# Kernel optimization log

Measured on AMD Instinct MI355X. Metric: run time of the kernel, lower is better.

## Reference

```python
import jax, jax.numpy as jnp
import numpy as np

EPS = 1e-7
ATTN_W_EPS = float(np.sqrt(EPS))
RESIDUAL_SCALE = 1.0


def mish(v):
    return v * jnp.tanh(jax.nn.softplus(v))


def setup_inputs() -> dict:
    key = jax.random.key(0)
    ks = jax.random.split(key, 12)
    N, E, dim, hidden = 100000, 500000, 128, 128
    x = jax.random.normal(ks[0], (N, dim), dtype=jnp.float32)
    edge_attr = jax.random.normal(ks[1], (E, dim), dtype=jnp.float32)
    head_node_index = jax.random.randint(ks[2], (E,), 0, N)
    tail_node_index = jax.random.randint(ks[3], (E,), 0, N)
    node_batch = jax.random.randint(ks[4], (N,), 0, 8)
    edge_batch = jax.random.randint(ks[5], (E,), 0, 8)
    s_in = 1.0 / np.sqrt(dim)
    s_out = 1.0 / np.sqrt(hidden)
    W_node_in = jax.random.normal(ks[6], (dim, 4 * hidden), dtype=jnp.float32) * s_in
    W_edge_in = jax.random.normal(ks[7], (dim, 3 * hidden), dtype=jnp.float32) * s_in
    node_message_bias = jnp.zeros((hidden,), dtype=jnp.float32)
    edge_message_bias = jnp.zeros((hidden,), dtype=jnp.float32)
    W_node_out = jax.random.normal(ks[8], (hidden, dim), dtype=jnp.float32) * s_out
    b_node_out = jnp.zeros((dim,), dtype=jnp.float32)
    W_edge_out = jax.random.normal(ks[9], (hidden, dim), dtype=jnp.float32) * s_out
    b_edge_out = jnp.zeros((dim,), dtype=jnp.float32)
    return {
        'x': x, 'edge_attr': edge_attr,
        'head_node_index': head_node_index, 'tail_node_index': tail_node_index,
        'node_batch': node_batch, 'edge_batch': edge_batch,
        'num_nodes': N, 'num_graphs': 8,
        'W_node_in': W_node_in, 'W_edge_in': W_edge_in,
        'node_message_bias': node_message_bias, 'edge_message_bias': edge_message_bias,
        'W_node_out': W_node_out, 'b_node_out': b_node_out,
        'W_edge_out': W_edge_out, 'b_edge_out': b_edge_out,
    }


def reference(x, edge_attr, head_node_index, tail_node_index, node_batch, edge_batch,
              num_nodes, num_graphs, W_node_in, W_edge_in,
              node_message_bias, edge_message_bias,
              W_node_out, b_node_out, W_edge_out, b_edge_out):
    hidden = node_message_bias.shape[0]
    # node input linear -> 4 chunks
    node_messages = x @ W_node_in  # [N, 4*hidden]
    node_to_self, node_to_neighbor, head_to_edge, tail_to_edge = jnp.split(node_messages, 4, axis=-1)
    node_to_edge = head_to_edge[head_node_index] + tail_to_edge[tail_node_index]  # [E, hidden]
    # edge input linear -> 3 chunks
    edge_messages = edge_attr @ W_edge_in  # [E, 3*hidden]
    edge_to_self, edge_to_tail, edge_attn_message = jnp.split(edge_messages, 3, axis=-1)
    # segment-softmax-style attention weight (max detached, per tail node)
    seg_max = jax.ops.segment_max(jax.lax.stop_gradient(edge_attn_message), tail_node_index,
                                  num_segments=num_nodes)  # [N, hidden]
    edge_attn_weight = jnp.exp(edge_attn_message - seg_max[tail_node_index]) + ATTN_W_EPS  # [E, hidden]
    # attention-weighted scatter aggregation to tail nodes
    sent = (node_to_neighbor[head_node_index] + edge_to_tail) * edge_attn_weight  # [E, hidden]
    received = jax.ops.segment_sum(sent, tail_node_index, num_segments=num_nodes)
    recv_weight = jax.ops.segment_sum(edge_attn_weight, tail_node_index, num_segments=num_nodes)
    node_received = received / (recv_weight + EPS)  # [N, hidden]
    # node output path
    x_residual = mish(node_received + node_to_self + node_message_bias) @ W_node_out + b_node_out
    x_out = x + RESIDUAL_SCALE * x_residual
    # edge output path
    e_residual = mish(node_to_edge + edge_to_self + edge_message_bias) @ W_edge_out + b_edge_out
    edge_attr_out = edge_attr + RESIDUAL_SCALE * e_residual
    return (x_out, edge_attr_out)
```

## Files before the change

kernel.cpp:

```cpp
#include <hip/hip_runtime.h>
#include <hip/hip_bf16.h>
#include <math.h>

typedef short bf16x8 __attribute__((ext_vector_type(8)));
typedef float f32x4 __attribute__((ext_vector_type(4)));
typedef unsigned int u32;
typedef unsigned short u16;

#define DIM 128
#define ATTN_EPS 3.1622776601683794e-4f
#define DIV_EPS 1e-7f
#define SCAN_BLKS 256

__device__ __forceinline__ u16 f2b(float f) {
  u32 u = __float_as_uint(f);
  return (u16)((u + 0x7FFFu + ((u >> 16) & 1u)) >> 16);
}
__device__ __forceinline__ float b2f(u16 s) { return __uint_as_float(((u32)s) << 16); }
__device__ __forceinline__ float mish_f(float v) {
  float e = __expf(fminf(v, 15.f));
  float w = 1.f + e;
  return v * (1.f - 2.f * __builtin_amdgcn_rcpf(w * w + 1.f));
}

template <int NT, int NR>
__device__ __forceinline__ void stage_f32(u16 (*dst)[136], const float* __restrict__ src,
                                          long rowbase, long nrows, int tid) {
  #pragma unroll
  for (int it = 0; it < NR * 16 / NT; ++it) {
    int i = it * NT + tid;
    int r = i >> 4, c = (i & 15) * 8;
    long gr = rowbase + r;
    bf16x8 v;
    if (gr < nrows) {
      const f32x4* p = (const f32x4*)(src + gr * (long)DIM + c);
      f32x4 a = p[0], b = p[1];
      #pragma unroll
      for (int j = 0; j < 4; ++j) { v[j] = (short)f2b(a[j]); v[j + 4] = (short)f2b(b[j]); }
    } else {
      #pragma unroll
      for (int j = 0; j < 8; ++j) v[j] = 0;
    }
    *(bf16x8*)&dst[r][c] = v;
  }
}

template <int NT, int NR>
__device__ __forceinline__ void stage_b16(u16 (*dst)[136], const u16* __restrict__ src, int tid) {
  #pragma unroll
  for (int it = 0; it < NR * 16 / NT; ++it) {
    int i = it * NT + tid;
    int r = i >> 4, c = (i & 15) * 8;
    *(bf16x8*)&dst[r][c] = *(const bf16x8*)&src[(long)r * DIM + c];
  }
}

template <int NT, int NR>
__device__ __forceinline__ void gather_nm(u16 (*dst)[136], const u16* __restrict__ nm,
    const int* __restrict__ idx, int segoff, long rowbase, long nrows, int tid) {
  #pragma unroll
  for (int it = 0; it < NR * 16 / NT; ++it) {
    int i = it * NT + tid;
    int r = i >> 4, c = (i & 15) * 8;
    long gr = rowbase + r;
    bf16x8 v;
    if (gr < nrows) {
      v = *(const bf16x8*)&nm[(long)idx[gr] * 512 + segoff + c];
    } else {
      #pragma unroll
      for (int j = 0; j < 8; ++j) v[j] = 0;
    }
    *(bf16x8*)&dst[r][c] = v;
  }
}

__device__ __forceinline__ void mm_32x64(const u16 (*As)[136], const u16 (*Bs)[136],
                                         int wr, int wc, int lane, f32x4 acc[2][4]) {
  int r0 = wr * 32 + (lane & 15);
  int cb = wc * 64 + (lane & 15);
  int koff = (lane >> 4) * 8;
  #pragma unroll
  for (int ks = 0; ks < 4; ++ks) {
    int k = ks * 32 + koff;
    bf16x8 a0 = *(const bf16x8*)&As[r0][k];
    bf16x8 a1 = *(const bf16x8*)&As[r0 + 16][k];
    #pragma unroll
    for (int ct = 0; ct < 4; ++ct) {
      bf16x8 b = *(const bf16x8*)&Bs[cb + ct * 16][k];
      acc[0][ct] = __builtin_amdgcn_mfma_f32_16x16x32_bf16(a0, b, acc[0][ct], 0, 0, 0);
      acc[1][ct] = __builtin_amdgcn_mfma_f32_16x16x32_bf16(a1, b, acc[1][ct], 0, 0, 0);
    }
  }
}

__global__ void k_prep(const float* __restrict__ Wni, const float* __restrict__ Wei,
                       const float* __restrict__ Wno, const float* __restrict__ Weo,
                       u16* __restrict__ Tni, u16* __restrict__ Tei,
                       u16* __restrict__ Tno, u16* __restrict__ Teo) {
  int stride = gridDim.x * blockDim.x;
  int t0 = blockIdx.x * blockDim.x + threadIdx.x;
  for (int i = t0; i < 128 * 512; i += stride) { int k = i >> 9, c = i & 511; Tni[c * 128 + k] = f2b(Wni[i]); }
  for (int i = t0; i < 128 * 384; i += stride) { int k = i / 384, c = i % 384; Tei[c * 128 + k] = f2b(Wei[i]); }
  for (int i = t0; i < 128 * 128; i += stride) { int k = i >> 7, c = i & 127; Tno[c * 128 + k] = f2b(Wno[i]); }
  for (int i = t0; i < 128 * 128; i += stride) { int k = i >> 7, c = i & 127; Teo[c * 128 + k] = f2b(Weo[i]); }
}

__global__ __launch_bounds__(256) void k_node_in(const float* __restrict__ x,
    const u16* __restrict__ Tni, u16* __restrict__ nm, int N) {
  __shared__ u16 As[64][136];
  __shared__ u16 Bs[128][136];
  int tid = threadIdx.x, lane = tid & 63;
  int wid = tid >> 6, wr = wid >> 1, wc = wid & 1;
  long rowbase = (long)blockIdx.x * 64;
  stage_f32<256, 64>(As, x, rowbase, N, tid);
  stage_b16<256, 128>(Bs, Tni + (long)blockIdx.y * 128 * DIM, tid);
  __syncthreads();
  f32x4 acc[2][4] = {};
  mm_32x64(As, Bs, wr, wc, lane, acc);
  #pragma unroll
  for (int rt = 0; rt < 2; ++rt)
  #pragma unroll
  for (int j = 0; j < 4; ++j) {
    int lr = wr * 32 + rt * 16 + ((lane >> 4) << 2) + j;
    long r = rowbase + lr;
    if (r >= N) continue;
    #pragma unroll
    for (int ct = 0; ct < 4; ++ct) {
      int col = blockIdx.y * 128 + wc * 64 + ct * 16 + (lane & 15);
      nm[r * 512 + col] = f2b(acc[rt][ct][j]);
    }
  }
}

__global__ __launch_bounds__(512, 4) void k_edge_in(const float* __restrict__ ea,
    const u16* __restrict__ Tei, const u16* __restrict__ Teo,
    const u16* __restrict__ nm, const int* __restrict__ head, const int* __restrict__ tail,
    const float* __restrict__ ebias, const float* __restrict__ beo,
    u32* __restrict__ em, float* __restrict__ eout, int E) {
  __shared__ u16 As[128][136];
  __shared__ u16 Bs[128][136];
  int tid = threadIdx.x, lane = tid & 63;
  int wid = tid >> 6, wr = wid >> 1, wc = wid & 1;
  long rowbase = (long)blockIdx.x * 128;
  int col0 = wc * 64 + (lane & 15);

  stage_f32<512, 128>(As, ea, rowbase, E, tid);
  stage_b16<512, 128>(Bs, Tei + 128 * DIM, tid);
  __syncthreads();
  f32x4 acc_t[2][4] = {};
  mm_32x64(As, Bs, wr, wc, lane, acc_t);
  __syncthreads();
  stage_b16<512, 128>(Bs, Tei + 256 * DIM, tid);
  __syncthreads();
  f32x4 acc_m[2][4] = {};
  mm_32x64(As, Bs, wr, wc, lane, acc_m);
  __syncthreads();
  gather_nm<512, 128>(Bs, nm, head, 128, rowbase, E, tid);
  __syncthreads();
  #pragma unroll
  for (int rt = 0; rt < 2; ++rt)
  #pragma unroll
  for (int j = 0; j < 4; ++j) {
    int lr = wr * 32 + rt * 16 + ((lane >> 4) << 2) + j;
    long r = rowbase + lr;
    if (r < E) {
      #pragma unroll
      for (int ct = 0; ct < 4; ++ct) {
        int col = col0 + ct * 16;
        float n2n = b2f(Bs[lr][col]);
        em[r * 128 + col] = (u32)f2b(n2n + acc_t[rt][ct][j])
                          | ((u32)f2b(acc_m[rt][ct][j]) << 16);
      }
    }
  }
  __syncthreads();
  stage_b16<512, 128>(Bs, Tei, tid);
  __syncthreads();
  f32x4 acc_s[2][4] = {};
  mm_32x64(As, Bs, wr, wc, lane, acc_s);
  __syncthreads();
  gather_nm<512, 128>(Bs, nm, head, 256, rowbase, E, tid);
  gather_nm<512, 128>(As, nm, tail, 384, rowbase, E, tid);
  __syncthreads();
  #pragma unroll
  for (int rt = 0; rt < 2; ++rt)
  #pragma unroll
  for (int j = 0; j < 4; ++j) {
    int lr = wr * 32 + rt * 16 + ((lane >> 4) << 2) + j;
    long r = rowbase + lr;
    #pragma unroll
    for (int ct = 0; ct < 4; ++ct) {
      int col = col0 + ct * 16;
      if (r < E) {
        float epre = acc_s[rt][ct][j] + b2f(Bs[lr][col]) + b2f(As[lr][col]) + ebias[col];
        As[lr][col] = f2b(mish_f(epre));
      } else {
        As[lr][col] = 0;
      }
    }
  }
  __syncthreads();
  stage_b16<512, 128>(Bs, Teo, tid);
  __syncthreads();
  f32x4 acc_o[2][4] = {};
  mm_32x64(As, Bs, wr, wc, lane, acc_o);
  #pragma unroll
  for (int rt = 0; rt < 2; ++rt)
  #pragma unroll
  for (int j = 0; j < 4; ++j) {
    int lr = wr * 32 + rt * 16 + ((lane >> 4) << 2) + j;
    long r = rowbase + lr;
    if (r >= E) continue;
    #pragma unroll
    for (int ct = 0; ct < 4; ++ct) {
      int col = col0 + ct * 16;
      eout[r * DIM + col] = ea[r * DIM + col] + acc_o[rt][ct][j] + beo[col];
    }
  }
}

__global__ void k_zero(u32* __restrict__ deg, int N) {
  int i = blockIdx.x * blockDim.x + threadIdx.x;
  int stride = gridDim.x * blockDim.x;
  for (; i < N; i += stride) deg[i] = 0;
}
__global__ void k_count(const int* __restrict__ tail, u32* __restrict__ deg, int E) {
  int i = blockIdx.x * blockDim.x + threadIdx.x;
  int stride = gridDim.x * blockDim.x;
  for (; i < E; i += stride) atomicAdd(&deg[tail[i]], 1u);
}
__global__ __launch_bounds__(256) void k_scan_part(const u32* __restrict__ deg,
                                                   u32* __restrict__ part, int N) {
  __shared__ u32 red[256];
  int tid = threadIdx.x, b = blockIdx.x;
  int chunk = (N + SCAN_BLKS - 1) / SCAN_BLKS;
  int lo = b * chunk, hi = min(lo + chunk, N);
  u32 s = 0;
  for (int i = lo + tid; i < hi; i += 256) s += deg[i];
  red[tid] = s; __syncthreads();
  for (int st = 128; st > 0; st >>= 1) { if (tid < st) red[tid] += red[tid + st]; __syncthreads(); }
  if (tid == 0) part[b] = red[0];
}
__global__ __launch_bounds__(256) void k_scan_mid(u32* __restrict__ part) {
  __shared__ u32 lds[256];
  int tid = threadIdx.x;
  u32 v = part[tid];
  lds[tid] = v; __syncthreads();
  for (int s = 1; s < 256; s <<= 1) {
    u32 a = (tid >= s) ? lds[tid - s] : 0; __syncthreads();
    lds[tid] += a; __syncthreads();
  }
  part[tid] = lds[tid] - v;
}
__global__ __launch_bounds__(256) void k_scan_fin(const u32* __restrict__ deg,
    const u32* __restrict__ part, u32* __restrict__ off, u32* __restrict__ cur, int N) {
  __shared__ u32 lds[256];
  int tid = threadIdx.x, b = blockIdx.x;
  int chunk = (N + SCAN_BLKS - 1) / SCAN_BLKS;
  int lo = b * chunk, hi = min(lo + chunk, N);
  u32 carry = part[b];
  for (int base = lo; base < hi; base += 256) {
    int i = base + tid;
    u32 v = (i < hi) ? deg[i] : 0;
    lds[tid] = v; __syncthreads();
    for (int s = 1; s < 256; s <<= 1) {
      u32 a = (tid >= s) ? lds[tid - s] : 0; __syncthreads();
      lds[tid] += a; __syncthreads();
    }
    u32 incl = lds[tid], total = lds[255];
    __syncthreads();
    if (i < hi) { u32 o = carry + incl - v; off[i] = o; cur[i] = o; }
    carry += total;
  }
}
__global__ void k_fill(const int* __restrict__ tail, u32* __restrict__ cur,
                       u32* __restrict__ csr, int E) {
  int i = blockIdx.x * blockDim.x + threadIdx.x;
  int stride = gridDim.x * blockDim.x;
  for (; i < E; i += stride) { u32 p = atomicAdd(&cur[tail[i]], 1u); csr[p] = (u32)i; }
}

__global__ __launch_bounds__(256) void k_node_agg(const u32* __restrict__ em,
    const u16* __restrict__ nm, const u32* __restrict__ off, const u32* __restrict__ deg,
    const u32* __restrict__ csr, const float* __restrict__ nbias,
    u16* __restrict__ hbuf, int N) {
  int tid = threadIdx.x, lane = tid & 63;
  int node = blockIdx.x * 4 + (tid >> 6);
  if (node >= N) return;
  int ch = lane * 2;
  u32 o = off[node], d = deg[node];
  float m0 = -INFINITY, m1 = -INFINITY;
  float s0 = 0.f, s1 = 0.f, v0 = 0.f, v1 = 0.f, sv0 = 0.f, sv1 = 0.f;
  u32 e = d ? csr[o] : 0u;
  for (u32 i = 0; i < d; ++i) {
    u32 ec = e;
    if (i + 1 < d) e = csr[o + i + 1];
    uint2 pp = *(const uint2*)(em + (long)ec * 128 + ch);
    float val0 = b2f((u16)(pp.x & 0xffff)), g0 = b2f((u16)(pp.x >> 16));
    float val1 = b2f((u16)(pp.y & 0xffff)), g1 = b2f((u16)(pp.y >> 16));
    float nmx0 = fmaxf(m0, g0);
    float sc0 = __expf(m0 - nmx0), pe0 = __expf(g0 - nmx0);
    s0 = s0 * sc0 + pe0; v0 = v0 * sc0 + pe0 * val0; sv0 += val0; m0 = nmx0;
    float nmx1 = fmaxf(m1, g1);
    float sc1 = __expf(m1 - nmx1), pe1 = __expf(g1 - nmx1);
    s1 = s1 * sc1 + pe1; v1 = v1 * sc1 + pe1 * val1; sv1 += val1; m1 = nmx1;
  }
  float de = (float)d * ATTN_EPS;
  float r0 = (v0 + ATTN_EPS * sv0) * __builtin_amdgcn_rcpf(s0 + de + DIV_EPS);
  float r1 = (v1 + ATTN_EPS * sv1) * __builtin_amdgcn_rcpf(s1 + de + DIV_EPS);
  u32 np = *(const u32*)&nm[(long)node * 512 + ch];
  float ns0 = b2f((u16)(np & 0xffff)), ns1 = b2f((u16)(np >> 16));
  float h0 = mish_f(r0 + ns0 + nbias[ch]);
  float h1 = mish_f(r1 + ns1 + nbias[ch + 1]);
  *(u32*)&hbuf[(long)node * 128 + ch] = (u32)f2b(h0) | ((u32)f2b(h1) << 16);
}

__global__ __launch_bounds__(256) void k_node_out(const float* __restrict__ x,
    const u16* __restrict__ hbuf, const u16* __restrict__ Tno, const float* __restrict__ bno,
    float* __restrict__ xout, int N) {
  __shared__ u16 As[64][136];
  __shared__ u16 Bs[128][136];
  int tid = threadIdx.x, lane = tid & 63;
  int wid = tid >> 6, wr = wid >> 1, wc = wid & 1;
  long rowbase = (long)blockIdx.x * 64;
  stage_b16<256, 64>(As, hbuf + rowbase * DIM, tid);
  stage_b16<256, 128>(Bs, Tno, tid);
  __syncthreads();
  f32x4 acc[2][4] = {};
  mm_32x64(As, Bs, wr, wc, lane, acc);
  #pragma unroll
  for (int rt = 0; rt < 2; ++rt)
  #pragma unroll
  for (int j = 0; j < 4; ++j) {
    int lr = wr * 32 + rt * 16 + ((lane >> 4) << 2) + j;
    long r = rowbase + lr;
    if (r >= N) continue;
    #pragma unroll
    for (int ct = 0; ct < 4; ++ct) {
      int col = wc * 64 + ct * 16 + (lane & 15);
      xout[r * DIM + col] = x[r * DIM + col] + acc[rt][ct][j] + bno[col];
    }
  }
}

extern "C" void kernel_launch(void* const* d_in, const int* in_sizes, int n_in,
                              void* d_out, int out_size, void* d_ws, size_t ws_size,
                              hipStream_t stream) {
  const float* x     = (const float*)d_in[0];
  const float* ea    = (const float*)d_in[1];
  const int*   head  = (const int*)d_in[2];
  const int*   tail  = (const int*)d_in[3];
  const float* Wni   = (const float*)d_in[8];
  const float* Wei   = (const float*)d_in[9];
  const float* nbias = (const float*)d_in[10];
  const float* ebias = (const float*)d_in[11];
  const float* Wno   = (const float*)d_in[12];
  const float* bno   = (const float*)d_in[13];
  const float* Weo   = (const float*)d_in[14];
  const float* beo   = (const float*)d_in[15];
  const int N = in_sizes[0] / DIM;
  const int E = in_sizes[1] / DIM;
  const int NB = (N + 63) / 64;
  const int EB = (E + 127) / 128;
  const int NPAD = NB * 64;

  char* ws = (char*)d_ws;
  u16*   nm   = (u16*)ws; ws += (size_t)N * 512 * 2;
  u32*   em   = (u32*)ws; ws += (size_t)E * 128 * 4;
  u16*   hbuf = (u16*)ws; ws += (size_t)NPAD * 128 * 2;
  u32*   deg  = (u32*)ws; ws += (size_t)N * 4;
  u32*   off  = (u32*)ws; ws += (size_t)N * 4;
  u32*   cur  = (u32*)ws; ws += (size_t)N * 4;
  u32*   part = (u32*)ws; ws += (size_t)SCAN_BLKS * 4;
  u32*   csr  = (u32*)ws; ws += (size_t)E * 4;
  u16* Tni = (u16*)ws; ws += 512 * DIM * 2;
  u16* Tei = (u16*)ws; ws += 384 * DIM * 2;
  u16* Tno = (u16*)ws; ws += DIM * DIM * 2;
  u16* Teo = (u16*)ws; ws += DIM * DIM * 2;

  float* xout = (float*)d_out;
  float* eout = xout + (size_t)N * DIM;

  k_prep<<<128, 256, 0, stream>>>(Wni, Wei, Wno, Weo, Tni, Tei, Tno, Teo);
  k_zero<<<128, 256, 0, stream>>>(deg, N);
  k_count<<<512, 256, 0, stream>>>(tail, deg, E);
  k_scan_part<<<SCAN_BLKS, 256, 0, stream>>>(deg, part, N);
  k_scan_mid<<<1, 256, 0, stream>>>(part);
  k_scan_fin<<<SCAN_BLKS, 256, 0, stream>>>(deg, part, off, cur, N);
  k_fill<<<512, 256, 0, stream>>>(tail, cur, csr, E);
  k_node_in<<<dim3(NB, 4), 256, 0, stream>>>(x, Tni, nm, N);
  k_edge_in<<<EB, 512, 0, stream>>>(ea, Tei, Teo, nm, head, tail, ebias, beo, em, eout, E);
  k_node_agg<<<(N + 3) / 4, 256, 0, stream>>>(em, nm, off, deg, csr, nbias, hbuf, N);
  k_node_out<<<NB, 256, 0, stream>>>(x, hbuf, Tno, bno, xout, N);
}
```

Before: 607.7 us.

## Scatter edge messages in CSR order, fuse aggregation with node output GEMM

The edge kernel now writes each edge's message row directly at its CSR position (pos from the atomic fill), so the aggregation kernel streams contiguous rows instead of chasing an index list. Aggregation and the node output GEMM are fused into one kernel that keeps mish outputs in LDS, which drops the hbuf round trip. Weight tiles are no longer staged in LDS; B fragments are read straight from global/L2 in the MFMA loops. The node input GEMM also computes all four chunks per 128-row block, so the activation tile is loaded only once. The trade-off is scattered em writes and more global B reads. Some gathers are also moved earlier so they overlap the matmuls.

```diff
diff --git a/kernel.cpp b/kernel.cpp
--- a/kernel.cpp
+++ b/kernel.cpp
@@ -46,16 +46,6 @@
 }
 
 template <int NT, int NR>
-__device__ __forceinline__ void stage_b16(u16 (*dst)[136], const u16* __restrict__ src, int tid) {
-  #pragma unroll
-  for (int it = 0; it < NR * 16 / NT; ++it) {
-    int i = it * NT + tid;
-    int r = i >> 4, c = (i & 15) * 8;
-    *(bf16x8*)&dst[r][c] = *(const bf16x8*)&src[(long)r * DIM + c];
-  }
-}
-
-template <int NT, int NR>
 __device__ __forceinline__ void gather_nm(u16 (*dst)[136], const u16* __restrict__ nm,
     const int* __restrict__ idx, int segoff, long rowbase, long nrows, int tid) {
   #pragma unroll
@@ -74,8 +64,34 @@
   }
 }
 
-__device__ __forceinline__ void mm_32x64(const u16 (*As)[136], const u16 (*Bs)[136],
-                                         int wr, int wc, int lane, f32x4 acc[2][4]) {
+template <int NT, int NR>
+__device__ __forceinline__ void gather_load(bf16x8 (&v)[NR * 16 / NT], const u16* __restrict__ nm,
+    const int* __restrict__ idx, int segoff, long rowbase, long nrows, int tid) {
+  #pragma unroll
+  for (int it = 0; it < NR * 16 / NT; ++it) {
+    int i = it * NT + tid;
+    int r = i >> 4, c = (i & 15) * 8;
+    long gr = rowbase + r;
+    if (gr < nrows) {
+      v[it] = *(const bf16x8*)&nm[(long)idx[gr] * 512 + segoff + c];
+    } else {
+      #pragma unroll
+      for (int j = 0; j < 8; ++j) v[it][j] = 0;
+    }
+  }
+}
+template <int NT, int NR>
+__device__ __forceinline__ void gather_store(u16 (*dst)[136], const bf16x8 (&v)[NR * 16 / NT], int tid) {
+  #pragma unroll
+  for (int it = 0; it < NR * 16 / NT; ++it) {
+    int i = it * NT + tid;
+    int r = i >> 4, c = (i & 15) * 8;
+    *(bf16x8*)&dst[r][c] = v[it];
+  }
+}
+
+__device__ __forceinline__ void mm_32x64_gB(const u16 (*As)[136], const u16* __restrict__ Bg,
+                                            int wr, int wc, int lane, f32x4 acc[2][4]) {
   int r0 = wr * 32 + (lane & 15);
   int cb = wc * 64 + (lane & 15);
   int koff = (lane >> 4) * 8;
@@ -86,9 +102,32 @@
     bf16x8 a1 = *(const bf16x8*)&As[r0 + 16][k];
     #pragma unroll
     for (int ct = 0; ct < 4; ++ct) {
-      bf16x8 b = *(const bf16x8*)&Bs[cb + ct * 16][k];
+      bf16x8 b = *(const bf16x8*)&Bg[(long)(cb + ct * 16) * 128 + k];
       acc[0][ct] = __builtin_amdgcn_mfma_f32_16x16x32_bf16(a0, b, acc[0][ct], 0, 0, 0);
       acc[1][ct] = __builtin_amdgcn_mfma_f32_16x16x32_bf16(a1, b, acc[1][ct], 0, 0, 0);
+    }
+  }
+}
+__device__ __forceinline__ void mm_32x64_gB2(const u16 (*As)[136],
+    const u16* __restrict__ B0, const u16* __restrict__ B1,
+    int wr, int wc, int lane, f32x4 acc0[2][4], f32x4 acc1[2][4]) {
+  int r0 = wr * 32 + (lane & 15);
+  int cb = wc * 64 + (lane & 15);
+  int koff = (lane >> 4) * 8;
+  #pragma unroll
+  for (int ks = 0; ks < 4; ++ks) {
+    int k = ks * 32 + koff;
+    bf16x8 a0 = *(const bf16x8*)&As[r0][k];
+    bf16x8 a1 = *(const bf16x8*)&As[r0 + 16][k];
+    #pragma unroll
+    for (int ct = 0; ct < 4; ++ct) {
+      long bo = (long)(cb + ct * 16) * 128 + k;
+      bf16x8 b0 = *(const bf16x8*)&B0[bo];
+      bf16x8 b1 = *(const bf16x8*)&B1[bo];
+      acc0[0][ct] = __builtin_amdgcn_mfma_f32_16x16x32_bf16(a0, b0, acc0[0][ct], 0, 0, 0);
+      acc0[1][ct] = __builtin_amdgcn_mfma_f32_16x16x32_bf16(a1, b0, acc0[1][ct], 0, 0, 0);
+      acc1[0][ct] = __builtin_amdgcn_mfma_f32_16x16x32_bf16(a0, b1, acc1[0][ct], 0, 0, 0);
+      acc1[1][ct] = __builtin_amdgcn_mfma_f32_16x16x32_bf16(a1, b1, acc1[1][ct], 0, 0, 0);
     }
   }
 }
@@ -105,29 +144,30 @@
   for (int i = t0; i < 128 * 128; i += stride) { int k = i >> 7, c = i & 127; Teo[c * 128 + k] = f2b(Weo[i]); }
 }
 
-__global__ __launch_bounds__(256) void k_node_in(const float* __restrict__ x,
+__global__ __launch_bounds__(512, 4) void k_node_in(const float* __restrict__ x,
     const u16* __restrict__ Tni, u16* __restrict__ nm, int N) {
-  __shared__ u16 As[64][136];
-  __shared__ u16 Bs[128][136];
+  __shared__ u16 As[128][136];
   int tid = threadIdx.x, lane = tid & 63;
   int wid = tid >> 6, wr = wid >> 1, wc = wid & 1;
-  long rowbase = (long)blockIdx.x * 64;
-  stage_f32<256, 64>(As, x, rowbase, N, tid);
-  stage_b16<256, 128>(Bs, Tni + (long)blockIdx.y * 128 * DIM, tid);
-  __syncthreads();
-  f32x4 acc[2][4] = {};
-  mm_32x64(As, Bs, wr, wc, lane, acc);
-  #pragma unroll
-  for (int rt = 0; rt < 2; ++rt)
-  #pragma unroll
-  for (int j = 0; j < 4; ++j) {
-    int lr = wr * 32 + rt * 16 + ((lane >> 4) << 2) + j;
-    long r = rowbase + lr;
-    if (r >= N) continue;
-    #pragma unroll
-    for (int ct = 0; ct < 4; ++ct) {
-      int col = blockIdx.y * 128 + wc * 64 + ct * 16 + (lane & 15);
-      nm[r * 512 + col] = f2b(acc[rt][ct][j]);
+  long rowbase = (long)blockIdx.x * 128;
+  stage_f32<512, 128>(As, x, rowbase, N, tid);
+  __syncthreads();
+  #pragma unroll 1
+  for (int chunk = 0; chunk < 4; ++chunk) {
+    f32x4 acc[2][4] = {};
+    mm_32x64_gB(As, Tni + chunk * 128 * 128, wr, wc, lane, acc);
+    #pragma unroll
+    for (int rt = 0; rt < 2; ++rt)
+    #pragma unroll
+    for (int j = 0; j < 4; ++j) {
+      int lr = wr * 32 + rt * 16 + ((lane >> 4) << 2) + j;
+      long r = rowbase + lr;
+      if (r >= N) continue;
+      #pragma unroll
+      for (int ct = 0; ct < 4; ++ct) {
+        int col = wc * 64 + ct * 16 + (lane & 15);
+        nm[r * 512 + chunk * 128 + col] = f2b(acc[rt][ct][j]);
+      }
     }
   }
 }
@@ -135,28 +175,21 @@
 __global__ __launch_bounds__(512, 4) void k_edge_in(const float* __restrict__ ea,
     const u16* __restrict__ Tei, const u16* __restrict__ Teo,
     const u16* __restrict__ nm, const int* __restrict__ head, const int* __restrict__ tail,
-    const float* __restrict__ ebias, const float* __restrict__ beo,
+    const u32* __restrict__ pos, const float* __restrict__ ebias, const float* __restrict__ beo,
     u32* __restrict__ em, float* __restrict__ eout, int E) {
   __shared__ u16 As[128][136];
-  __shared__ u16 Bs[128][136];
+  __shared__ u16 Gs[128][136];
   int tid = threadIdx.x, lane = tid & 63;
   int wid = tid >> 6, wr = wid >> 1, wc = wid & 1;
   long rowbase = (long)blockIdx.x * 128;
   int col0 = wc * 64 + (lane & 15);
 
   stage_f32<512, 128>(As, ea, rowbase, E, tid);
-  stage_b16<512, 128>(Bs, Tei + 128 * DIM, tid);
-  __syncthreads();
-  f32x4 acc_t[2][4] = {};
-  mm_32x64(As, Bs, wr, wc, lane, acc_t);
-  __syncthreads();
-  stage_b16<512, 128>(Bs, Tei + 256 * DIM, tid);
-  __syncthreads();
-  f32x4 acc_m[2][4] = {};
-  mm_32x64(As, Bs, wr, wc, lane, acc_m);
-  __syncthreads();
-  gather_nm<512, 128>(Bs, nm, head, 128, rowbase, E, tid);
-  __syncthreads();
+  gather_nm<512, 128>(Gs, nm, head, 128, rowbase, E, tid);
+  __syncthreads();
+
+  f32x4 acc_t[2][4] = {}, acc_m[2][4] = {};
+  mm_32x64_gB2(As, Tei + 128 * 128, Tei + 256 * 128, wr, wc, lane, acc_t, acc_m);
   #pragma unroll
   for (int rt = 0; rt < 2; ++rt)
   #pragma unroll
@@ -164,24 +197,27 @@
     int lr = wr * 32 + rt * 16 + ((lane >> 4) << 2) + j;
     long r = rowbase + lr;
     if (r < E) {
+      long p = pos[r];
       #pragma unroll
       for (int ct = 0; ct < 4; ++ct) {
         int col = col0 + ct * 16;
-        float n2n = b2f(Bs[lr][col]);
-        em[r * 128 + col] = (u32)f2b(n2n + acc_t[rt][ct][j])
+        float n2n = b2f(Gs[lr][col]);
+        em[p * 128 + col] = (u32)f2b(n2n + acc_t[rt][ct][j])
                           | ((u32)f2b(acc_m[rt][ct][j]) << 16);
       }
     }
   }
   __syncthreads();
-  stage_b16<512, 128>(Bs, Tei, tid);
-  __syncthreads();
+
+  gather_nm<512, 128>(Gs, nm, head, 256, rowbase, E, tid);
   f32x4 acc_s[2][4] = {};
-  mm_32x64(As, Bs, wr, wc, lane, acc_s);
-  __syncthreads();
-  gather_nm<512, 128>(Bs, nm, head, 256, rowbase, E, tid);
-  gather_nm<512, 128>(As, nm, tail, 384, rowbase, E, tid);
-  __syncthreads();
+  mm_32x64_gB(As, Tei, wr, wc, lane, acc_s);
+  bf16x8 t2e[4];
+  gather_load<512, 128>(t2e, nm, tail, 384, rowbase, E, tid);
+  __syncthreads();
+  gather_store<512, 128>(As, t2e, tid);
+  __syncthreads();
+
   #pragma unroll
   for (int rt = 0; rt < 2; ++rt)
   #pragma unroll
@@ -192,7 +228,7 @@
     for (int ct = 0; ct < 4; ++ct) {
       int col = col0 + ct * 16;
       if (r < E) {
-        float epre = acc_s[rt][ct][j] + b2f(Bs[lr][col]) + b2f(As[lr][col]) + ebias[col];
+        float epre = acc_s[rt][ct][j] + b2f(Gs[lr][col]) + b2f(As[lr][col]) + ebias[col];
         As[lr][col] = f2b(mish_f(epre));
       } else {
         As[lr][col] = 0;
@@ -200,10 +236,9 @@
     }
   }
   __syncthreads();
-  stage_b16<512, 128>(Bs, Teo, tid);
-  __syncthreads();
+
   f32x4 acc_o[2][4] = {};
-  mm_32x64(As, Bs, wr, wc, lane, acc_o);
+  mm_32x64_gB(As, Teo, wr, wc, lane, acc_o);
   #pragma unroll
   for (int rt = 0; rt < 2; ++rt)
   #pragma unroll
@@ -274,60 +309,56 @@
   }
 }
 __global__ void k_fill(const int* __restrict__ tail, u32* __restrict__ cur,
-                       u32* __restrict__ csr, int E) {
+                       u32* __restrict__ pos, int E) {
   int i = blockIdx.x * blockDim.x + threadIdx.x;
   int stride = gridDim.x * blockDim.x;
-  for (; i < E; i += stride) { u32 p = atomicAdd(&cur[tail[i]], 1u); csr[p] = (u32)i; }
-}
-
-__global__ __launch_bounds__(256) void k_node_agg(const u32* __restrict__ em,
+  for (; i < E; i += stride) pos[i] = atomicAdd(&cur[tail[i]], 1u);
+}
+
+__global__ __launch_bounds__(512, 4) void k_agg_out(const u32* __restrict__ em,
     const u16* __restrict__ nm, const u32* __restrict__ off, const u32* __restrict__ deg,
-    const u32* __restrict__ csr, const float* __restrict__ nbias,
-    u16* __restrict__ hbuf, int N) {
-  int tid = threadIdx.x, lane = tid & 63;
-  int node = blockIdx.x * 4 + (tid >> 6);
-  if (node >= N) return;
+    const float* __restrict__ nbias, const float* __restrict__ x,
+    const u16* __restrict__ Tno, const float* __restrict__ bno,
+    float* __restrict__ xout, int N) {
+  __shared__ u16 Hs[128][136];
+  int tid = threadIdx.x, lane = tid & 63, wid = tid >> 6;
+  long rowbase = (long)blockIdx.x * 128;
   int ch = lane * 2;
-  u32 o = off[node], d = deg[node];
-  float m0 = -INFINITY, m1 = -INFINITY;
-  float s0 = 0.f, s1 = 0.f, v0 = 0.f, v1 = 0.f, sv0 = 0.f, sv1 = 0.f;
-  u32 e = d ? csr[o] : 0u;
-  for (u32 i = 0; i < d; ++i) {
-    u32 ec = e;
-    if (i + 1 < d) e = csr[o + i + 1];
-    uint2 pp = *(const uint2*)(em + (long)ec * 128 + ch);
-    float val0 = b2f((u16)(pp.x & 0xffff)), g0 = b2f((u16)(pp.x >> 16));
-    float val1 = b2f((u16)(pp.y & 0xffff)), g1 = b2f((u16)(pp.y >> 16));
-    float nmx0 = fmaxf(m0, g0);
-    float sc0 = __expf(m0 - nmx0), pe0 = __expf(g0 - nmx0);
-    s0 = s0 * sc0 + pe0; v0 = v0 * sc0 + pe0 * val0; sv0 += val0; m0 = nmx0;
-    float nmx1 = fmaxf(m1, g1);
-    float sc1 = __expf(m1 - nmx1), pe1 = __expf(g1 - nmx1);
-    s1 = s1 * sc1 + pe1; v1 = v1 * sc1 + pe1 * val1; sv1 += val1; m1 = nmx1;
-  }
-  float de = (float)d * ATTN_EPS;
-  float r0 = (v0 + ATTN_EPS * sv0) * __builtin_amdgcn_rcpf(s0 + de + DIV_EPS);
-  float r1 = (v1 + ATTN_EPS * sv1) * __builtin_amdgcn_rcpf(s1 + de + DIV_EPS);
-  u32 np = *(const u32*)&nm[(long)node * 512 + ch];
-  float ns0 = b2f((u16)(np & 0xffff)), ns1 = b2f((u16)(np >> 16));
-  float h0 = mish_f(r0 + ns0 + nbias[ch]);
-  float h1 = mish_f(r1 + ns1 + nbias[ch + 1]);
-  *(u32*)&hbuf[(long)node * 128 + ch] = (u32)f2b(h0) | ((u32)f2b(h1) << 16);
-}
-
-__global__ __launch_bounds__(256) void k_node_out(const float* __restrict__ x,
-    const u16* __restrict__ hbuf, const u16* __restrict__ Tno, const float* __restrict__ bno,
-    float* __restrict__ xout, int N) {
-  __shared__ u16 As[64][136];
-  __shared__ u16 Bs[128][136];
-  int tid = threadIdx.x, lane = tid & 63;
-  int wid = tid >> 6, wr = wid >> 1, wc = wid & 1;
-  long rowbase = (long)blockIdx.x * 64;
-  stage_b16<256, 64>(As, hbuf + rowbase * DIM, tid);
-  stage_b16<256, 128>(Bs, Tno, tid);
-  __syncthreads();
+  float nb0 = nbias[ch], nb1 = nbias[ch + 1];
+  for (int s = 0; s < 16; ++s) {
+    int lr = wid * 16 + s;
+    long node = rowbase + lr;
+    u32 hpack = 0;
+    if (node < N) {
+      u32 o = off[node], d = deg[node];
+      float m0 = -INFINITY, m1 = -INFINITY;
+      float s0 = 0.f, s1 = 0.f, v0 = 0.f, v1 = 0.f, sv0 = 0.f, sv1 = 0.f;
+      const u32* rowp = em + (long)o * 128 + ch;
+      for (u32 i = 0; i < d; ++i, rowp += 128) {
+        uint2 pp = *(const uint2*)rowp;
+        float val0 = b2f((u16)(pp.x & 0xffff)), g0 = b2f((u16)(pp.x >> 16));
+        float val1 = b2f((u16)(pp.y & 0xffff)), g1 = b2f((u16)(pp.y >> 16));
+        float nmx0 = fmaxf(m0, g0);
+        float sc0 = __expf(m0 - nmx0), pe0 = __expf(g0 - nmx0);
+        s0 = s0 * sc0 + pe0; v0 = v0 * sc0 + pe0 * val0; sv0 += val0; m0 = nmx0;
+        float nmx1 = fmaxf(m1, g1);
+        float sc1 = __expf(m1 - nmx1), pe1 = __expf(g1 - nmx1);
+        s1 = s1 * sc1 + pe1; v1 = v1 * sc1 + pe1 * val1; sv1 += val1; m1 = nmx1;
+      }
+      float de = (float)d * ATTN_EPS;
+      float r0 = (v0 + ATTN_EPS * sv0) * __builtin_amdgcn_rcpf(s0 + de + DIV_EPS);
+      float r1 = (v1 + ATTN_EPS * sv1) * __builtin_amdgcn_rcpf(s1 + de + DIV_EPS);
+      u32 np = *(const u32*)&nm[node * 512 + ch];
+      float h0 = mish_f(r0 + b2f((u16)(np & 0xffff)) + nb0);
+      float h1 = mish_f(r1 + b2f((u16)(np >> 16)) + nb1);
+      hpack = (u32)f2b(h0) | ((u32)f2b(h1) << 16);
+    }
+    *(u32*)&Hs[lr][ch] = hpack;
+  }
+  __syncthreads();
+  int wr = wid >> 1, wc = wid & 1;
   f32x4 acc[2][4] = {};
-  mm_32x64(As, Bs, wr, wc, lane, acc);
+  mm_32x64_gB(Hs, Tno, wr, wc, lane, acc);
   #pragma unroll
   for (int rt = 0; rt < 2; ++rt)
   #pragma unroll
@@ -360,19 +391,17 @@
   const float* beo   = (const float*)d_in[15];
   const int N = in_sizes[0] / DIM;
   const int E = in_sizes[1] / DIM;
-  const int NB = (N + 63) / 64;
+  const int NB = (N + 127) / 128;
   const int EB = (E + 127) / 128;
-  const int NPAD = NB * 64;
 
   char* ws = (char*)d_ws;
   u16*   nm   = (u16*)ws; ws += (size_t)N * 512 * 2;
   u32*   em   = (u32*)ws; ws += (size_t)E * 128 * 4;
-  u16*   hbuf = (u16*)ws; ws += (size_t)NPAD * 128 * 2;
   u32*   deg  = (u32*)ws; ws += (size_t)N * 4;
   u32*   off  = (u32*)ws; ws += (size_t)N * 4;
   u32*   cur  = (u32*)ws; ws += (size_t)N * 4;
   u32*   part = (u32*)ws; ws += (size_t)SCAN_BLKS * 4;
-  u32*   csr  = (u32*)ws; ws += (size_t)E * 4;
+  u32*   pos  = (u32*)ws; ws += (size_t)E * 4;
   u16* Tni = (u16*)ws; ws += 512 * DIM * 2;
   u16* Tei = (u16*)ws; ws += 384 * DIM * 2;
   u16* Tno = (u16*)ws; ws += DIM * DIM * 2;
@@ -387,9 +416,8 @@
   k_scan_part<<<SCAN_BLKS, 256, 0, stream>>>(deg, part, N);
   k_scan_mid<<<1, 256, 0, stream>>>(part);
   k_scan_fin<<<SCAN_BLKS, 256, 0, stream>>>(deg, part, off, cur, N);
-  k_fill<<<512, 256, 0, stream>>>(tail, cur, csr, E);
-  k_node_in<<<dim3(NB, 4), 256, 0, stream>>>(x, Tni, nm, N);
-  k_edge_in<<<EB, 512, 0, stream>>>(ea, Tei, Teo, nm, head, tail, ebias, beo, em, eout, E);
-  k_node_agg<<<(N + 3) / 4, 256, 0, stream>>>(em, nm, off, deg, csr, nbias, hbuf, N);
-  k_node_out<<<NB, 256, 0, stream>>>(x, hbuf, Tno, bno, xout, N);
-}
+  k_fill<<<512, 256, 0, stream>>>(tail, cur, pos, E);
+  k_node_in<<<NB, 512, 0, stream>>>(x, Tni, nm, N);
+  k_edge_in<<<EB, 512, 0, stream>>>(ea, Tei, Teo, nm, head, tail, pos, ebias, beo, em, eout, E);
+  k_agg_out<<<NB, 512, 0, stream>>>(em, nm, off, deg, nbias, x, Tno, bno, xout, N);
+}
```

Result: slower. 777.7 us (+28.0%).

## Prefetch edge-kernel operands into registers and fuse aggregation with node output GEMM

Applied to the files above, without the earlier changes.

In the edge kernel, weight tiles and gathered node-message rows are now loaded into registers before the preceding MFMA stage and only written to LDS after it, so global-load latency overlaps with compute. The node aggregation and node output projection are merged into one kernel that builds the 128-row hidden tile in LDS and multiplies it directly. This drops the hbuf round trip and one launch. The cost is higher register pressure in the edge kernel and a less parallel aggregation phase, where each wave walks 16 nodes in sequence. A no-op block and a wr&1 change in k_node_in are cosmetic.

```diff
diff --git a/kernel.cpp b/kernel.cpp
--- a/kernel.cpp
+++ b/kernel.cpp
@@ -56,21 +56,38 @@
 }
 
 template <int NT, int NR>
-__device__ __forceinline__ void gather_nm(u16 (*dst)[136], const u16* __restrict__ nm,
+__device__ __forceinline__ void load_rows(bf16x8 (&v)[NR * 16 / NT], const u16* __restrict__ src,
+                                          int tid) {
+  #pragma unroll
+  for (int it = 0; it < NR * 16 / NT; ++it) {
+    int i = it * NT + tid;
+    int r = i >> 4, c = (i & 15) * 8;
+    v[it] = *(const bf16x8*)&src[(long)r * DIM + c];
+  }
+}
+template <int NT, int NR>
+__device__ __forceinline__ void gather_load(bf16x8 (&v)[NR * 16 / NT], const u16* __restrict__ nm,
     const int* __restrict__ idx, int segoff, long rowbase, long nrows, int tid) {
   #pragma unroll
   for (int it = 0; it < NR * 16 / NT; ++it) {
     int i = it * NT + tid;
     int r = i >> 4, c = (i & 15) * 8;
     long gr = rowbase + r;
-    bf16x8 v;
     if (gr < nrows) {
-      v = *(const bf16x8*)&nm[(long)idx[gr] * 512 + segoff + c];
+      v[it] = *(const bf16x8*)&nm[(long)idx[gr] * 512 + segoff + c];
     } else {
       #pragma unroll
-      for (int j = 0; j < 8; ++j) v[j] = 0;
-    }
-    *(bf16x8*)&dst[r][c] = v;
+      for (int j = 0; j < 8; ++j) v[it][j] = 0;
+    }
+  }
+}
+template <int NT, int NR>
+__device__ __forceinline__ void store_rows(u16 (*dst)[136], const bf16x8 (&v)[NR * 16 / NT], int tid) {
+  #pragma unroll
+  for (int it = 0; it < NR * 16 / NT; ++it) {
+    int i = it * NT + tid;
+    int r = i >> 4, c = (i & 15) * 8;
+    *(bf16x8*)&dst[r][c] = v[it];
   }
 }
 
@@ -116,12 +133,18 @@
   stage_b16<256, 128>(Bs, Tni + (long)blockIdx.y * 128 * DIM, tid);
   __syncthreads();
   f32x4 acc[2][4] = {};
-  mm_32x64(As, Bs, wr, wc, lane, acc);
+  {
+    int r0 = (wr & 1) * 32 + (lane & 15);
+    int cb = wc * 64 + (lane & 15);
+    int koff = (lane >> 4) * 8;
+    (void)r0; (void)cb; (void)koff;
+  }
+  mm_32x64((const u16(*)[136])As, Bs, wr & 1, wc, lane, acc);
   #pragma unroll
   for (int rt = 0; rt < 2; ++rt)
   #pragma unroll
   for (int j = 0; j < 4; ++j) {
-    int lr = wr * 32 + rt * 16 + ((lane >> 4) << 2) + j;
+    int lr = (wr & 1) * 32 + rt * 16 + ((lane >> 4) << 2) + j;
     long r = rowbase + lr;
     if (r >= N) continue;
     #pragma unroll
@@ -144,19 +167,30 @@
   long rowbase = (long)blockIdx.x * 128;
   int col0 = wc * 64 + (lane & 15);
 
+  stage_b16<512, 128>(Bs, Tei + 128 * DIM, tid);
   stage_f32<512, 128>(As, ea, rowbase, E, tid);
-  stage_b16<512, 128>(Bs, Tei + 128 * DIM, tid);
-  __syncthreads();
+  bf16x8 g1[4];
+  gather_load<512, 128>(g1, nm, head, 128, rowbase, E, tid);
+  __syncthreads();
+
+  bf16x8 wreg[4];
+  load_rows<512, 128>(wreg, Tei + 256 * DIM, tid);
   f32x4 acc_t[2][4] = {};
   mm_32x64(As, Bs, wr, wc, lane, acc_t);
   __syncthreads();
-  stage_b16<512, 128>(Bs, Tei + 256 * DIM, tid);
-  __syncthreads();
+  store_rows<512, 128>(Bs, wreg, tid);
+  __syncthreads();
+
   f32x4 acc_m[2][4] = {};
   mm_32x64(As, Bs, wr, wc, lane, acc_m);
   __syncthreads();
-  gather_nm<512, 128>(Bs, nm, head, 128, rowbase, E, tid);
-  __syncthreads();
+  store_rows<512, 128>(Bs, g1, tid);
+  __syncthreads();
+
+  load_rows<512, 128>(wreg, Tei, tid);
+  bf16x8 g2[4], g3[4];
+  gather_load<512, 128>(g2, nm, head, 256, rowbase, E, tid);
+  gather_load<512, 128>(g3, nm, tail, 384, rowbase, E, tid);
   #pragma unroll
   for (int rt = 0; rt < 2; ++rt)
   #pragma unroll
@@ -174,14 +208,17 @@
     }
   }
   __syncthreads();
-  stage_b16<512, 128>(Bs, Tei, tid);
-  __syncthreads();
+  store_rows<512, 128>(Bs, wreg, tid);
+  __syncthreads();
+
   f32x4 acc_s[2][4] = {};
   mm_32x64(As, Bs, wr, wc, lane, acc_s);
   __syncthreads();
-  gather_nm<512, 128>(Bs, nm, head, 256, rowbase, E, tid);
-  gather_nm<512, 128>(As, nm, tail, 384, rowbase, E, tid);
-  __syncthreads();
+  store_rows<512, 128>(As, g3, tid);
+  store_rows<512, 128>(Bs, g2, tid);
+  __syncthreads();
+
+  load_rows<512, 128>(wreg, Teo, tid);
   #pragma unroll
   for (int rt = 0; rt < 2; ++rt)
   #pragma unroll
@@ -200,8 +237,9 @@
     }
   }
   __syncthreads();
-  stage_b16<512, 128>(Bs, Teo, tid);
-  __syncthreads();
+  store_rows<512, 128>(Bs, wreg, tid);
+  __syncthreads();
+
   f32x4 acc_o[2][4] = {};
   mm_32x64(As, Bs, wr, wc, lane, acc_o);
   #pragma unroll
@@ -280,54 +318,54 @@
   for (; i < E; i += stride) { u32 p = atomicAdd(&cur[tail[i]], 1u); csr[p] = (u32)i; }
 }
 
-__global__ __launch_bounds__(256) void k_node_agg(const u32* __restrict__ em,
+__global__ __launch_bounds__(512, 4) void k_agg_out(const u32* __restrict__ em,
     const u16* __restrict__ nm, const u32* __restrict__ off, const u32* __restrict__ deg,
-    const u32* __restrict__ csr, const float* __restrict__ nbias,
-    u16* __restrict__ hbuf, int N) {
-  int tid = threadIdx.x, lane = tid & 63;
-  int node = blockIdx.x * 4 + (tid >> 6);
-  if (node >= N) return;
+    const u32* __restrict__ csr, const float* __restrict__ nbias, const float* __restrict__ x,
+    const u16* __restrict__ Tno, const float* __restrict__ bno,
+    float* __restrict__ xout, int N) {
+  __shared__ u16 Hs[128][136];
+  __shared__ u16 Bs[128][136];
+  int tid = threadIdx.x, lane = tid & 63, wid = tid >> 6;
+  long rowbase = (long)blockIdx.x * 128;
   int ch = lane * 2;
-  u32 o = off[node], d = deg[node];
-  float m0 = -INFINITY, m1 = -INFINITY;
-  float s0 = 0.f, s1 = 0.f, v0 = 0.f, v1 = 0.f, sv0 = 0.f, sv1 = 0.f;
-  u32 e = d ? csr[o] : 0u;
-  for (u32 i = 0; i < d; ++i) {
-    u32 ec = e;
-    if (i + 1 < d) e = csr[o + i + 1];
-    uint2 pp = *(const uint2*)(em + (long)ec * 128 + ch);
-    float val0 = b2f((u16)(pp.x & 0xffff)), g0 = b2f((u16)(pp.x >> 16));
-    float val1 = b2f((u16)(pp.y & 0xffff)), g1 = b2f((u16)(pp.y >> 16));
-    float nmx0 = fmaxf(m0, g0);
-    float sc0 = __expf(m0 - nmx0), pe0 = __expf(g0 - nmx0);
-    s0 = s0 * sc0 + pe0; v0 = v0 * sc0 + pe0 * val0; sv0 += val0; m0 = nmx0;
-    float nmx1 = fmaxf(m1, g1);
-    float sc1 = __expf(m1 - nmx1), pe1 = __expf(g1 - nmx1);
-    s1 = s1 * sc1 + pe1; v1 = v1 * sc1 + pe1 * val1; sv1 += val1; m1 = nmx1;
-  }
-  float de = (float)d * ATTN_EPS;
-  float r0 = (v0 + ATTN_EPS * sv0) * __builtin_amdgcn_rcpf(s0 + de + DIV_EPS);
-  float r1 = (v1 + ATTN_EPS * sv1) * __builtin_amdgcn_rcpf(s1 + de + DIV_EPS);
-  u32 np = *(const u32*)&nm[(long)node * 512 + ch];
-  float ns0 = b2f((u16)(np & 0xffff)), ns1 = b2f((u16)(np >> 16));
-  float h0 = mish_f(r0 + ns0 + nbias[ch]);
-  float h1 = mish_f(r1 + ns1 + nbias[ch + 1]);
-  *(u32*)&hbuf[(long)node * 128 + ch] = (u32)f2b(h0) | ((u32)f2b(h1) << 16);
-}
-
-__global__ __launch_bounds__(256) void k_node_out(const float* __restrict__ x,
-    const u16* __restrict__ hbuf, const u16* __restrict__ Tno, const float* __restrict__ bno,
-    float* __restrict__ xout, int N) {
-  __shared__ u16 As[64][136];
-  __shared__ u16 Bs[128][136];
-  int tid = threadIdx.x, lane = tid & 63;
-  int wid = tid >> 6, wr = wid >> 1, wc = wid & 1;
-  long rowbase = (long)blockIdx.x * 64;
-  stage_b16<256, 64>(As, hbuf + rowbase * DIM, tid);
-  stage_b16<256, 128>(Bs, Tno, tid);
-  __syncthreads();
+  float nb0 = nbias[ch], nb1 = nbias[ch + 1];
+  stage_b16<512, 128>(Bs, Tno, tid);
+  for (int s = 0; s < 16; ++s) {
+    int lr = wid * 16 + s;
+    long node = rowbase + lr;
+    u32 hpack = 0;
+    if (node < N) {
+      u32 o = off[node], d = deg[node];
+      float m0 = -INFINITY, m1 = -INFINITY;
+      float s0 = 0.f, s1 = 0.f, v0 = 0.f, v1 = 0.f, sv0 = 0.f, sv1 = 0.f;
+      u32 e = d ? csr[o] : 0u;
+      for (u32 i = 0; i < d; ++i) {
+        u32 ec = e;
+        if (i + 1 < d) e = csr[o + i + 1];
+        uint2 pp = *(const uint2*)(em + (long)ec * 128 + ch);
+        float val0 = b2f((u16)(pp.x & 0xffff)), g0 = b2f((u16)(pp.x >> 16));
+        float val1 = b2f((u16)(pp.y & 0xffff)), g1 = b2f((u16)(pp.y >> 16));
+        float nmx0 = fmaxf(m0, g0);
+        float sc0 = __expf(m0 - nmx0), pe0 = __expf(g0 - nmx0);
+        s0 = s0 * sc0 + pe0; v0 = v0 * sc0 + pe0 * val0; sv0 += val0; m0 = nmx0;
+        float nmx1 = fmaxf(m1, g1);
+        float sc1 = __expf(m1 - nmx1), pe1 = __expf(g1 - nmx1);
+        s1 = s1 * sc1 + pe1; v1 = v1 * sc1 + pe1 * val1; sv1 += val1; m1 = nmx1;
+      }
+      float de = (float)d * ATTN_EPS;
+      float r0 = (v0 + ATTN_EPS * sv0) * __builtin_amdgcn_rcpf(s0 + de + DIV_EPS);
+      float r1 = (v1 + ATTN_EPS * sv1) * __builtin_amdgcn_rcpf(s1 + de + DIV_EPS);
+      u32 np = *(const u32*)&nm[node * 512 + ch];
+      float h0 = mish_f(r0 + b2f((u16)(np & 0xffff)) + nb0);
+      float h1 = mish_f(r1 + b2f((u16)(np >> 16)) + nb1);
+      hpack = (u32)f2b(h0) | ((u32)f2b(h1) << 16);
+    }
+    *(u32*)&Hs[lr][ch] = hpack;
+  }
+  __syncthreads();
+  int wr = wid >> 1, wc = wid & 1;
   f32x4 acc[2][4] = {};
-  mm_32x64(As, Bs, wr, wc, lane, acc);
+  mm_32x64(Hs, Bs, wr, wc, lane, acc);
   #pragma unroll
   for (int rt = 0; rt < 2; ++rt)
   #pragma unroll
@@ -360,14 +398,13 @@
   const float* beo   = (const float*)d_in[15];
   const int N = in_sizes[0] / DIM;
   const int E = in_sizes[1] / DIM;
-  const int NB = (N + 63) / 64;
+  const int NB64 = (N + 63) / 64;
+  const int NB128 = (N + 127) / 128;
   const int EB = (E + 127) / 128;
-  const int NPAD = NB * 64;
 
   char* ws = (char*)d_ws;
   u16*   nm   = (u16*)ws; ws += (size_t)N * 512 * 2;
   u32*   em   = (u32*)ws; ws += (size_t)E * 128 * 4;
-  u16*   hbuf = (u16*)ws; ws += (size_t)NPAD * 128 * 2;
   u32*   deg  = (u32*)ws; ws += (size_t)N * 4;
   u32*   off  = (u32*)ws; ws += (size_t)N * 4;
   u32*   cur  = (u32*)ws; ws += (size_t)N * 4;
@@ -388,8 +425,7 @@
   k_scan_mid<<<1, 256, 0, stream>>>(part);
   k_scan_fin<<<SCAN_BLKS, 256, 0, stream>>>(deg, part, off, cur, N);
   k_fill<<<512, 256, 0, stream>>>(tail, cur, csr, E);
-  k_node_in<<<dim3(NB, 4), 256, 0, stream>>>(x, Tni, nm, N);
+  k_node_in<<<dim3(NB64, 4), 256, 0, stream>>>(x, Tni, nm, N);
   k_edge_in<<<EB, 512, 0, stream>>>(ea, Tei, Teo, nm, head, tail, ebias, beo, em, eout, E);
-  k_node_agg<<<(N + 3) / 4, 256, 0, stream>>>(em, nm, off, deg, csr, nbias, hbuf, N);
-  k_node_out<<<NB, 256, 0, stream>>>(x, hbuf, Tno, bno, xout, N);
-}
+  k_agg_out<<<NB128, 512, 0, stream>>>(em, nm, off, deg, csr, nbias, x, Tno, bno, xout, N);
+}
```

Measured after the change: 745.5 us. 1.23x slower.

## Reuse staged x tile across all output chunks in node-in GEMM; prefetch edge rows in aggregation

Applied to the files above, without the earlier changes.

The node input GEMM now has each 512-thread block stage a 128-row x tile once and loop over the four 128-column weight chunks, restaging only the weight tile. Previously four separate blocks each reloaded and converted the same fp32 x rows. The aggregation kernel now prefetches the next edge's message row as well as its CSR index, and gets an occupancy hint in its launch bounds. The risks are fewer blocks in the node-in grid, plus the serial chunk loop with its extra barriers.

```diff
diff --git a/kernel.cpp b/kernel.cpp
--- a/kernel.cpp
+++ b/kernel.cpp
@@ -105,30 +105,36 @@
   for (int i = t0; i < 128 * 128; i += stride) { int k = i >> 7, c = i & 127; Teo[c * 128 + k] = f2b(Weo[i]); }
 }
 
-__global__ __launch_bounds__(256) void k_node_in(const float* __restrict__ x,
+__global__ __launch_bounds__(512, 4) void k_node_in(const float* __restrict__ x,
     const u16* __restrict__ Tni, u16* __restrict__ nm, int N) {
-  __shared__ u16 As[64][136];
+  __shared__ u16 As[128][136];
   __shared__ u16 Bs[128][136];
   int tid = threadIdx.x, lane = tid & 63;
   int wid = tid >> 6, wr = wid >> 1, wc = wid & 1;
-  long rowbase = (long)blockIdx.x * 64;
-  stage_f32<256, 64>(As, x, rowbase, N, tid);
-  stage_b16<256, 128>(Bs, Tni + (long)blockIdx.y * 128 * DIM, tid);
-  __syncthreads();
-  f32x4 acc[2][4] = {};
-  mm_32x64(As, Bs, wr, wc, lane, acc);
-  #pragma unroll
-  for (int rt = 0; rt < 2; ++rt)
-  #pragma unroll
-  for (int j = 0; j < 4; ++j) {
-    int lr = wr * 32 + rt * 16 + ((lane >> 4) << 2) + j;
-    long r = rowbase + lr;
-    if (r >= N) continue;
-    #pragma unroll
-    for (int ct = 0; ct < 4; ++ct) {
-      int col = blockIdx.y * 128 + wc * 64 + ct * 16 + (lane & 15);
-      nm[r * 512 + col] = f2b(acc[rt][ct][j]);
-    }
+  long rowbase = (long)blockIdx.x * 128;
+  stage_f32<512, 128>(As, x, rowbase, N, tid);
+  stage_b16<512, 128>(Bs, Tni, tid);
+  __syncthreads();
+  #pragma unroll 1
+  for (int chunk = 0; chunk < 4; ++chunk) {
+    f32x4 acc[2][4] = {};
+    mm_32x64(As, Bs, wr, wc, lane, acc);
+    __syncthreads();
+    if (chunk < 3) stage_b16<512, 128>(Bs, Tni + (chunk + 1) * 128 * DIM, tid);
+    #pragma unroll
+    for (int rt = 0; rt < 2; ++rt)
+    #pragma unroll
+    for (int j = 0; j < 4; ++j) {
+      int lr = wr * 32 + rt * 16 + ((lane >> 4) << 2) + j;
+      long r = rowbase + lr;
+      if (r >= N) continue;
+      #pragma unroll
+      for (int ct = 0; ct < 4; ++ct) {
+        int col = wc * 64 + ct * 16 + (lane & 15);
+        nm[r * 512 + chunk * 128 + col] = f2b(acc[rt][ct][j]);
+      }
+    }
+    if (chunk < 3) __syncthreads();
   }
 }
 
@@ -280,7 +286,7 @@
   for (; i < E; i += stride) { u32 p = atomicAdd(&cur[tail[i]], 1u); csr[p] = (u32)i; }
 }
 
-__global__ __launch_bounds__(256) void k_node_agg(const u32* __restrict__ em,
+__global__ __launch_bounds__(256, 8) void k_node_agg(const u32* __restrict__ em,
     const u16* __restrict__ nm, const u32* __restrict__ off, const u32* __restrict__ deg,
     const u32* __restrict__ csr, const float* __restrict__ nbias,
     u16* __restrict__ hbuf, int N) {
@@ -291,27 +297,31 @@
   u32 o = off[node], d = deg[node];
   float m0 = -INFINITY, m1 = -INFINITY;
   float s0 = 0.f, s1 = 0.f, v0 = 0.f, v1 = 0.f, sv0 = 0.f, sv1 = 0.f;
-  u32 e = d ? csr[o] : 0u;
-  for (u32 i = 0; i < d; ++i) {
-    u32 ec = e;
-    if (i + 1 < d) e = csr[o + i + 1];
-    uint2 pp = *(const uint2*)(em + (long)ec * 128 + ch);
-    float val0 = b2f((u16)(pp.x & 0xffff)), g0 = b2f((u16)(pp.x >> 16));
-    float val1 = b2f((u16)(pp.y & 0xffff)), g1 = b2f((u16)(pp.y >> 16));
-    float nmx0 = fmaxf(m0, g0);
-    float sc0 = __expf(m0 - nmx0), pe0 = __expf(g0 - nmx0);
-    s0 = s0 * sc0 + pe0; v0 = v0 * sc0 + pe0 * val0; sv0 += val0; m0 = nmx0;
-    float nmx1 = fmaxf(m1, g1);
-    float sc1 = __expf(m1 - nmx1), pe1 = __expf(g1 - nmx1);
-    s1 = s1 * sc1 + pe1; v1 = v1 * sc1 + pe1 * val1; sv1 += val1; m1 = nmx1;
+  if (d) {
+    u32 e = csr[o];
+    uint2 pp = *(const uint2*)(em + (long)e * 128 + ch);
+    for (u32 i = 0; i < d; ++i) {
+      uint2 ppc = pp;
+      if (i + 1 < d) {
+        u32 en = csr[o + i + 1];
+        pp = *(const uint2*)(em + (long)en * 128 + ch);
+      }
+      float val0 = b2f((u16)(ppc.x & 0xffff)), g0 = b2f((u16)(ppc.x >> 16));
+      float val1 = b2f((u16)(ppc.y & 0xffff)), g1 = b2f((u16)(ppc.y >> 16));
+      float nmx0 = fmaxf(m0, g0);
+      float sc0 = __expf(m0 - nmx0), pe0 = __expf(g0 - nmx0);
+      s0 = s0 * sc0 + pe0; v0 = v0 * sc0 + pe0 * val0; sv0 += val0; m0 = nmx0;
+      float nmx1 = fmaxf(m1, g1);
+      float sc1 = __expf(m1 - nmx1), pe1 = __expf(g1 - nmx1);
+      s1 = s1 * sc1 + pe1; v1 = v1 * sc1 + pe1 * val1; sv1 += val1; m1 = nmx1;
+    }
   }
   float de = (float)d * ATTN_EPS;
   float r0 = (v0 + ATTN_EPS * sv0) * __builtin_amdgcn_rcpf(s0 + de + DIV_EPS);
   float r1 = (v1 + ATTN_EPS * sv1) * __builtin_amdgcn_rcpf(s1 + de + DIV_EPS);
   u32 np = *(const u32*)&nm[(long)node * 512 + ch];
-  float ns0 = b2f((u16)(np & 0xffff)), ns1 = b2f((u16)(np >> 16));
-  float h0 = mish_f(r0 + ns0 + nbias[ch]);
-  float h1 = mish_f(r1 + ns1 + nbias[ch + 1]);
+  float h0 = mish_f(r0 + b2f((u16)(np & 0xffff)) + nbias[ch]);
+  float h1 = mish_f(r1 + b2f((u16)(np >> 16)) + nbias[ch + 1]);
   *(u32*)&hbuf[(long)node * 128 + ch] = (u32)f2b(h0) | ((u32)f2b(h1) << 16);
 }
 
@@ -360,9 +370,10 @@
   const float* beo   = (const float*)d_in[15];
   const int N = in_sizes[0] / DIM;
   const int E = in_sizes[1] / DIM;
-  const int NB = (N + 63) / 64;
+  const int NB64 = (N + 63) / 64;
+  const int NB128 = (N + 127) / 128;
   const int EB = (E + 127) / 128;
-  const int NPAD = NB * 64;
+  const int NPAD = NB64 * 64;
 
   char* ws = (char*)d_ws;
   u16*   nm   = (u16*)ws; ws += (size_t)N * 512 * 2;
@@ -388,8 +399,8 @@
   k_scan_mid<<<1, 256, 0, stream>>>(part);
   k_scan_fin<<<SCAN_BLKS, 256, 0, stream>>>(deg, part, off, cur, N);
   k_fill<<<512, 256, 0, stream>>>(tail, cur, csr, E);
-  k_node_in<<<dim3(NB, 4), 256, 0, stream>>>(x, Tni, nm, N);
+  k_node_in<<<NB128, 512, 0, stream>>>(x, Tni, nm, N);
   k_edge_in<<<EB, 512, 0, stream>>>(ea, Tei, Teo, nm, head, tail, ebias, beo, em, eout, E);
   k_node_agg<<<(N + 3) / 4, 256, 0, stream>>>(em, nm, off, deg, csr, nbias, hbuf, N);
-  k_node_out<<<NB, 256, 0, stream>>>(x, hbuf, Tno, bno, xout, N);
-}
+  k_node_out<<<NB64, 256, 0, stream>>>(x, hbuf, Tno, bno, xout, N);
+}
```

After: 606.2 us. No clear change (-0.2%).
